# Kernel optimization log

Hardware: AMD Instinct MI355X
Metric: run time of the kernel (lower is better)

## Reference

```python
import jax, jax.numpy as jnp
import numpy as np

H, KVH, DH = 16, 4, 64
DIM = 1024
SCALE_BASE = 4096  # context_len
EPS = 1e-6


def rmsnorm(x, g):
    return x * jax.lax.rsqrt(jnp.mean(x * x, axis=-1, keepdims=True) + EPS) * g


def rope_tables(n, dh, dtype):
    inv_freq = 1.0 / (10000.0 ** (jnp.arange(0, dh, 2, dtype=jnp.float32) / dh))
    t = jnp.arange(n, dtype=jnp.float32) * (SCALE_BASE / n)
    freqs = t[:, None] * inv_freq[None, :]          # [n, dh/2]
    emb = jnp.concatenate([freqs, freqs], axis=-1)  # [n, dh]
    return jnp.cos(emb).astype(dtype), jnp.sin(emb).astype(dtype)


def apply_rope(x, cos, sin):
    # x: [b, h, n, dh]; cos/sin: [n, dh]
    x1, x2 = jnp.split(x, 2, axis=-1)
    rot = jnp.concatenate([-x2, x1], axis=-1)
    return x * cos + rot * sin


def setup_inputs() -> dict:
    key = jax.random.key(0)
    ks = jax.random.split(key, 12)
    B, N = 1, 2048
    std = 0.02
    inp = {
        "x": jax.random.normal(ks[0], (B, N, DIM), jnp.float32),
        "a": jax.random.normal(ks[1], (B, N, DIM), jnp.float32),
        "g_x": jnp.ones((DIM,), jnp.float32),
        "g_a": jnp.ones((DIM,), jnp.float32),
        "Wq_x": jax.random.normal(ks[2], (DIM, H * DH), jnp.float32) * std,
        "Wkv_x": jax.random.normal(ks[3], (DIM, 2 * KVH * DH), jnp.float32) * std,
        "Wq_a": jax.random.normal(ks[4], (DIM, H * DH), jnp.float32) * std,
        "Wkv_a": jax.random.normal(ks[5], (DIM, 2 * KVH * DH), jnp.float32) * std,
        "Wout_x": jax.random.normal(ks[6], (H * DH, DIM), jnp.float32) * std,
        "bout_x": jnp.zeros((DIM,), jnp.float32),
        "Wout_a": jax.random.normal(ks[7], (H * DH, DIM), jnp.float32) * std,
        "bout_a": jnp.zeros((DIM,), jnp.float32),
    }
    return inp


def _split_heads(t, h):
    b, n, hd = t.shape
    return t.reshape(b, n, h, hd // h).transpose(0, 2, 1, 3)  # b h n d


def _stream_qkv(s, g, Wq, Wkv):
    s = rmsnorm(s, g)
    q = _split_heads(s @ Wq, H)                 # [b, H, n, DH]
    kv = s @ Wkv
    k, v = jnp.split(kv, 2, axis=-1)
    k = _split_heads(k, KVH)                    # [b, KVH, n, DH]
    v = _split_heads(v, KVH)
    return q, k, v


def reference(x, a, g_x, g_a, Wq_x, Wkv_x, Wq_a, Wkv_a, Wout_x, bout_x, Wout_a, bout_a):
    B, Nx, _ = x.shape
    Na = a.shape[1]
    scale = DH ** -0.5
    r = H // KVH

    q_x, k_x, v_x = _stream_qkv(x, g_x, Wq_x, Wkv_x)
    q_a, k_a, v_a = _stream_qkv(a, g_a, Wq_a, Wkv_a)

    cos_x, sin_x = rope_tables(Nx, DH, x.dtype)
    cos_a, sin_a = rope_tables(Na, DH, a.dtype)
    q_x, k_x = apply_rope(q_x, cos_x, sin_x), apply_rope(k_x, cos_x, sin_x)
    q_a, k_a = apply_rope(q_a, cos_a, sin_a), apply_rope(k_a, cos_a, sin_a)

    # NOTE: original scales q by dim_head**-0.5 AND sdpa scales again -> 1/DH total
    q_x = q_x * scale
    q_a = q_a * scale

    # GQA expansion: einops 'b h n d -> b (r h) n d' == tile heads
    tile = lambda t: jnp.tile(t, (1, r, 1, 1))
    k_x, v_x, k_a, v_a = tile(k_x), tile(v_x), tile(k_a), tile(v_a)

    # pack [a, x] along seq
    q = jnp.concatenate([q_a, q_x], axis=2)
    k = jnp.concatenate([k_a, k_x], axis=2)
    v = jnp.concatenate([v_a, v_x], axis=2)

    scores = jnp.einsum('bhqd,bhkd->bhqk', q, k) * scale  # sdpa's own scale
    attn = jax.nn.softmax(scores, axis=-1)
    out = jnp.einsum('bhqk,bhkd->bhqd', attn, v)          # [b, H, Na+Nx, DH]

    out_a, out_x = out[:, :, :Na], out[:, :, Na:]
    merge = lambda t: t.transpose(0, 2, 1, 3).reshape(B, -1, H * DH)
    out_x = merge(out_x) @ Wout_x + bout_x
    out_a = merge(out_a) @ Wout_a + bout_a
    return out_x, out_a
```

## Files before the change

### kernel.cpp

```cpp
#include <hip/hip_runtime.h>
#include <hip/hip_bf16.h>
#include <stdint.h>
#include <math.h>


#define NSEQ 2048
#define NJ   4096
#define DIMM 1024
#define LPAD 72

typedef __attribute__((ext_vector_type(4))) float f32x4;
typedef __attribute__((ext_vector_type(8))) short bf16x8;
typedef __attribute__((ext_vector_type(4))) short bf16x4;

__device__ __forceinline__ unsigned short f2bf(float f) {
  union { float f; uint32_t u; } v; v.f = f;
  return (unsigned short)((v.u + 0x7FFFu + ((v.u >> 16) & 1u)) >> 16);
}

__device__ __forceinline__ uint32_t pack2bf(float a, float b) {
  __hip_bfloat162 h = __float22bfloat162_rn(float2{a, b});
  union { __hip_bfloat162 h; uint32_t u; } c; c.h = h;
  return c.u;
}

#if defined(__has_builtin)
#if __has_builtin(__builtin_amdgcn_exp2f)
#define FAST_EXP2(x) __builtin_amdgcn_exp2f(x)
#endif
#endif
#ifndef FAST_EXP2
#define FAST_EXP2(x) exp2f(x)
#endif

__device__ __forceinline__ void glds16(const void* g, void* l) {
  __builtin_amdgcn_global_load_lds(
      (const __attribute__((address_space(1))) unsigned int*)g,
      (__attribute__((address_space(3))) unsigned int*)l, 16, 0, 0);
}

__global__ __launch_bounds__(256) void prep_kernel(
    const float* __restrict__ xa, const float* __restrict__ xx,
    const float* __restrict__ ga, const float* __restrict__ gx,
    const float* __restrict__ wqa, const float* __restrict__ wqx,
    const float* __restrict__ wkva, const float* __restrict__ wkvx,
    const float* __restrict__ woa, const float* __restrict__ wox,
    unsigned short* __restrict__ XN, unsigned short* __restrict__ WQT,
    unsigned short* __restrict__ WKVT, unsigned short* __restrict__ WOT,
    float* __restrict__ cosT, float* __restrict__ sinT) {
  __shared__ float tile[32][33];
  __shared__ float red[4];
  int bid = blockIdx.x, t = threadIdx.x;
  if (bid < 256) {
    int idx = bid * 256 + t;
    int pos = idx >> 5, i = idx & 31;
    double inv = pow(10000.0, -(double)i / 32.0);
    double ang = (double)(2 * pos) * inv;
    cosT[idx] = (float)cos(ang);
    sinT[idx] = (float)sin(ang);
  } else if (bid < 6400) {
    int b = bid - 256;
    int z = b >> 10, yx = b & 1023;
    int n0 = (yx >> 5) * 32, k0 = (yx & 31) * 32;
    int s = z & 1, ty = z >> 1;
    int N = (ty == 1) ? 512 : 1024;
    if (n0 >= N) return;
    const float* src = (z == 0) ? wqa : (z == 1) ? wqx : (z == 2) ? wkva
                     : (z == 3) ? wkvx : (z == 4) ? woa : wox;
    unsigned short* dst = (ty == 0) ? WQT + (size_t)s * 1024 * 1024
                        : (ty == 1) ? WKVT + (size_t)s * 512 * 1024
                                    : WOT + (size_t)s * 1024 * 1024;
    int r = t >> 3, c4 = (t & 7) * 4;
    f32x4 v = *(const f32x4*)(src + (size_t)(k0 + r) * N + n0 + c4);
    tile[r][c4 + 0] = v.x; tile[r][c4 + 1] = v.y;
    tile[r][c4 + 2] = v.z; tile[r][c4 + 3] = v.w;
    __syncthreads();
    int nn = t >> 3, kk = (t & 7) * 4;
    bf16x4 o;
    o.x = (short)f2bf(tile[kk + 0][nn]);
    o.y = (short)f2bf(tile[kk + 1][nn]);
    o.z = (short)f2bf(tile[kk + 2][nn]);
    o.w = (short)f2bf(tile[kk + 3][nn]);
    *(bf16x4*)(dst + (size_t)(n0 + nn) * 1024 + k0 + kk) = o;
  } else {
    int b = bid - 6400;
    int s = b >> 11, row = b & 2047;
    const float* src = (s == 0 ? xa : xx) + (size_t)row * DIMM;
    const float* g = (s == 0 ? ga : gx);
    f32x4 v = *(const f32x4*)(src + t * 4);
    float ss = v.x * v.x + v.y * v.y + v.z * v.z + v.w * v.w;
#pragma unroll
    for (int o = 32; o > 0; o >>= 1) ss += __shfl_xor(ss, o, 64);
    if ((t & 63) == 0) red[t >> 6] = ss;
    __syncthreads();
    float tot = red[0] + red[1] + red[2] + red[3];
    float rs = rsqrtf(tot * (1.0f / DIMM) + 1e-6f);
    f32x4 gv = *(const f32x4*)(g + t * 4);
    bf16x4 o;
    o.x = (short)f2bf(v.x * rs * gv.x);
    o.y = (short)f2bf(v.y * rs * gv.y);
    o.z = (short)f2bf(v.z * rs * gv.z);
    o.w = (short)f2bf(v.w * rs * gv.w);
    *(bf16x4*)(XN + ((size_t)s * NSEQ + row) * DIMM + t * 4) = o;
  }
}

__device__ __forceinline__ void gemm128_mainloop(
    const unsigned short* __restrict__ Ag, const unsigned short* __restrict__ Bg,
    unsigned short* As, unsigned short* Bs, f32x4 acc[4][4]) {
  int t = threadIdx.x;
  int lane = t & 63, wid = t >> 6;
  int wm = (wid >> 1) * 64, wn = (wid & 1) * 64;
  int l15 = lane & 15, quad = lane >> 4;
  int srow = t >> 2, sko = (t & 3) * 8;
  const unsigned short* ga = Ag + (size_t)srow * 1024 + sko;
  const unsigned short* gb = Bg + (size_t)srow * 1024 + sko;
  unsigned short* la = As + t * 8;
  unsigned short* lb = Bs + t * 8;
#pragma unroll
  for (int mi = 0; mi < 4; ++mi)
#pragma unroll
    for (int j = 0; j < 4; ++j) acc[mi][j] = (f32x4){0.f, 0.f, 0.f, 0.f};
  for (int kt = 0; kt < 32; ++kt) {
    int k0 = kt * 32;
    __syncthreads();
    glds16(ga + k0, la);
    glds16(ga + 64 * 1024 + k0, la + 2048);
    glds16(gb + k0, lb);
    glds16(gb + 64 * 1024 + k0, lb + 2048);
    __syncthreads();
    bf16x8 af[4], bfr[4];
#pragma unroll
    for (int mi = 0; mi < 4; ++mi)
      af[mi] = *(const bf16x8*)(As + (wm + mi * 16 + l15) * 32 + quad * 8);
#pragma unroll
    for (int j = 0; j < 4; ++j)
      bfr[j] = *(const bf16x8*)(Bs + (wn + j * 16 + l15) * 32 + quad * 8);
#pragma unroll
    for (int mi = 0; mi < 4; ++mi)
#pragma unroll
      for (int j = 0; j < 4; ++j)
        acc[mi][j] = __builtin_amdgcn_mfma_f32_16x16x32_bf16(af[mi], bfr[j],
                                                             acc[mi][j], 0, 0, 0);
  }
}

__global__ __launch_bounds__(256) void gemm_qkv_kernel(
    const unsigned short* __restrict__ XN, const unsigned short* __restrict__ WQT,
    const unsigned short* __restrict__ WKVT, const float* __restrict__ cosT,
    const float* __restrict__ sinT, unsigned short* __restrict__ QB,
    unsigned short* __restrict__ KB, unsigned short* __restrict__ VT) {
  __shared__ unsigned short As[128 * 32], Bs[128 * 32];
  int n0 = blockIdx.x * 128, m0 = blockIdx.y * 128;
  int s = (m0 >= 2048) ? 1 : 0;
  const unsigned short* Ag = XN + (size_t)m0 * 1024;
  const unsigned short* Bg = (n0 < 1024)
      ? WQT + (size_t)s * 1024 * 1024 + (size_t)n0 * 1024
      : WKVT + (size_t)s * 512 * 1024 + (size_t)(n0 - 1024) * 1024;
  f32x4 acc[4][4];
  gemm128_mainloop(Ag, Bg, As, Bs, acc);
  int t = threadIdx.x, lane = t & 63, wid = t >> 6;
  int wm = (wid >> 1) * 64, wn = (wid & 1) * 64;
  int l15 = lane & 15, quad = lane >> 4;
  int coln = n0 + wn;
  if (coln < 1280) {
    bool isq = coln < 1024;
    float sc = isq ? (1.4426950408889634f / 64.0f) : 1.0f;
    unsigned short* dstBase;
    if (isq) dstBase = QB + (size_t)(coln >> 6) * NJ * 64;
    else     dstBase = KB + (size_t)((coln - 1024) >> 6) * NJ * 64;
#pragma unroll
    for (int mi = 0; mi < 4; ++mi)
#pragma unroll
      for (int r = 0; r < 4; ++r) {
        int jr = m0 + wm + mi * 16 + quad * 4 + r;
        int pos = jr & 2047;
#pragma unroll
        for (int jp = 0; jp < 2; ++jp) {
          int i = jp * 16 + l15;
          float c = cosT[pos * 32 + i], sn = sinT[pos * 32 + i];
          float x1 = acc[mi][jp][r], x2 = acc[mi][jp + 2][r];
          dstBase[(size_t)jr * 64 + jp * 16 + l15]      = f2bf((x1 * c - x2 * sn) * sc);
          dstBase[(size_t)jr * 64 + 32 + jp * 16 + l15] = f2bf((x2 * c + x1 * sn) * sc);
        }
      }
  } else {
    int cvb = coln - 1280;
#pragma unroll
    for (int mi = 0; mi < 4; ++mi)
#pragma unroll
      for (int j = 0; j < 4; ++j) {
        int d = cvb + j * 16 + l15;
        int jr0 = m0 + wm + mi * 16 + quad * 4;
        union { bf16x4 v; uint32_t u[2]; } pv;
        pv.u[0] = pack2bf(acc[mi][j][0], acc[mi][j][1]);
        pv.u[1] = pack2bf(acc[mi][j][2], acc[mi][j][3]);
        *(bf16x4*)(VT + (size_t)d * NJ + jr0) = pv.v;
      }
  }
}

__global__ __launch_bounds__(256, 4) void attn_kernel(
    const unsigned short* __restrict__ QB, const unsigned short* __restrict__ KB,
    const unsigned short* __restrict__ VT, unsigned short* __restrict__ AT) {
  __shared__ unsigned short Ks[2][64 * LPAD];
  __shared__ unsigned short Vs[2][64 * LPAD];
  int h = blockIdx.y, qt = blockIdx.x;
  int hk = h & 3;
  int t = threadIdx.x, lane = t & 63, w = t >> 6;
  int l15 = lane & 15, quad = lane >> 4;
  int q0 = qt * 128 + w * 16;
  bf16x8 qf[2][2];
#pragma unroll
  for (int mi = 0; mi < 2; ++mi) {
    const unsigned short* qp = QB + ((size_t)h * NJ + q0 + mi * 64 + l15) * 64;
    qf[mi][0] = *(const bf16x8*)(qp + quad * 8);
    qf[mi][1] = *(const bf16x8*)(qp + 32 + quad * 8);
  }
  f32x4 oT[2][4];
  f32x4 oL[2];
#pragma unroll
  for (int mi = 0; mi < 2; ++mi) {
    oL[mi] = (f32x4){0.f, 0.f, 0.f, 0.f};
#pragma unroll
    for (int db = 0; db < 4; ++db) oT[mi][db] = (f32x4){0.f, 0.f, 0.f, 0.f};
  }
  bf16x8 vone;
  {
    short one = (l15 == 0) ? (short)0x3F80 : (short)0;
    vone = (bf16x8){one, one, one, one, one, one, one, one};
  }
  const unsigned short* Kg = KB + (size_t)hk * NJ * 64;
  const unsigned short* Vg = VT + (size_t)hk * 64 * NJ;
  int ky = t >> 3, dof = (t & 7) * 8;
  int pky = (ky & 0x23) | ((ky & 0x18) >> 1) | ((ky & 0x04) << 2);
  const unsigned short* KgA = Kg + (size_t)ky * 64 + dof;
  const unsigned short* KgB = Kg + (size_t)(32 + ky) * 64 + dof;
  const unsigned short* VgA = Vg + (size_t)ky * NJ + dof;
  const unsigned short* VgB = Vg + (size_t)(32 + ky) * NJ + dof;
  bf16x8 kr0 = *(const bf16x8*)(KgA);
  bf16x8 kr1 = *(const bf16x8*)(KgB);
  bf16x8 vr0 = *(const bf16x8*)(VgA);
  bf16x8 vr1 = *(const bf16x8*)(VgB);
  *(bf16x8*)(Ks[0] + pky * LPAD + dof) = kr0;
  *(bf16x8*)(Ks[0] + (32 + pky) * LPAD + dof) = kr1;
  *(bf16x8*)(Vs[0] + ky * LPAD + dof) = vr0;
  *(bf16x8*)(Vs[0] + (32 + ky) * LPAD + dof) = vr1;
  kr0 = *(const bf16x8*)(KgA + 4096);
  kr1 = *(const bf16x8*)(KgB + 4096);
  vr0 = *(const bf16x8*)(VgA + 64);
  vr1 = *(const bf16x8*)(VgB + 64);
  __syncthreads();
  for (int kt = 0; kt < 64; ++kt) {
    int cur = kt & 1;
    unsigned short* Kd = Ks[cur ^ 1];
    unsigned short* Vd = Vs[cur ^ 1];
    *(bf16x8*)(Kd + pky * LPAD + dof) = kr0;
    *(bf16x8*)(Kd + (32 + pky) * LPAD + dof) = kr1;
    *(bf16x8*)(Vd + ky * LPAD + dof) = vr0;
    *(bf16x8*)(Vd + (32 + ky) * LPAD + dof) = vr1;
    int tn = (kt + 2) & 63;
    kr0 = *(const bf16x8*)(KgA + (size_t)tn * 4096);
    kr1 = *(const bf16x8*)(KgB + (size_t)tn * 4096);
    vr0 = *(const bf16x8*)(VgA + tn * 64);
    vr1 = *(const bf16x8*)(VgB + tn * 64);
    const unsigned short* Kc = Ks[cur];
    const unsigned short* Vc = Vs[cur];
    f32x4 sx[2][4];
#pragma unroll
    for (int jb = 0; jb < 4; ++jb) {
      const unsigned short* kp = Kc + (jb * 16 + l15) * LPAD;
      bf16x8 kf0 = *(const bf16x8*)(kp + quad * 8);
      bf16x8 kf1 = *(const bf16x8*)(kp + 32 + quad * 8);
      f32x4 z0 = (f32x4){0.f, 0.f, 0.f, 0.f};
      z0 = __builtin_amdgcn_mfma_f32_16x16x32_bf16(kf0, qf[0][0], z0, 0, 0, 0);
      z0 = __builtin_amdgcn_mfma_f32_16x16x32_bf16(kf1, qf[0][1], z0, 0, 0, 0);
      sx[0][jb] = z0;
      f32x4 z1 = (f32x4){0.f, 0.f, 0.f, 0.f};
      z1 = __builtin_amdgcn_mfma_f32_16x16x32_bf16(kf0, qf[1][0], z1, 0, 0, 0);
      z1 = __builtin_amdgcn_mfma_f32_16x16x32_bf16(kf1, qf[1][1], z1, 0, 0, 0);
      sx[1][jb] = z1;
    }
    bf16x8 pb[2][2];
#pragma unroll
    for (int mi = 0; mi < 2; ++mi)
#pragma unroll
      for (int sb = 0; sb < 2; ++sb) {
        union { bf16x8 v; uint32_t u[4]; } pk;
        pk.u[0] = pack2bf(FAST_EXP2(sx[mi][2 * sb][0]), FAST_EXP2(sx[mi][2 * sb][1]));
        pk.u[1] = pack2bf(FAST_EXP2(sx[mi][2 * sb][2]), FAST_EXP2(sx[mi][2 * sb][3]));
        pk.u[2] = pack2bf(FAST_EXP2(sx[mi][2 * sb + 1][0]), FAST_EXP2(sx[mi][2 * sb + 1][1]));
        pk.u[3] = pack2bf(FAST_EXP2(sx[mi][2 * sb + 1][2]), FAST_EXP2(sx[mi][2 * sb + 1][3]));
        pb[mi][sb] = pk.v;
      }
#pragma unroll
    for (int db = 0; db < 4; ++db)
#pragma unroll
      for (int sb = 0; sb < 2; ++sb) {
        bf16x8 va = *(const bf16x8*)(Vc + (db * 16 + l15) * LPAD + sb * 32 + quad * 8);
        oT[0][db] = __builtin_amdgcn_mfma_f32_16x16x32_bf16(va, pb[0][sb],
                                                            oT[0][db], 0, 0, 0);
        oT[1][db] = __builtin_amdgcn_mfma_f32_16x16x32_bf16(va, pb[1][sb],
                                                            oT[1][db], 0, 0, 0);
      }
#pragma unroll
    for (int mi = 0; mi < 2; ++mi)
#pragma unroll
      for (int sb = 0; sb < 2; ++sb)
        oL[mi] = __builtin_amdgcn_mfma_f32_16x16x32_bf16(vone, pb[mi][sb],
                                                         oL[mi], 0, 0, 0);
    __syncthreads();
  }
#pragma unroll
  for (int mi = 0; mi < 2; ++mi) {
    float s = oL[mi][0];
    s += __shfl_xor(s, 16, 64);
    s += __shfl_xor(s, 32, 64);
    float inv = 1.0f / s;
    int qrow = q0 + mi * 64 + l15;
#pragma unroll
    for (int db = 0; db < 4; ++db) {
      union { bf16x4 v; uint32_t u[2]; } ov;
      ov.u[0] = pack2bf(oT[mi][db][0] * inv, oT[mi][db][1] * inv);
      ov.u[1] = pack2bf(oT[mi][db][2] * inv, oT[mi][db][3] * inv);
      *(bf16x4*)(AT + (size_t)qrow * DIMM + h * 64 + db * 16 + quad * 4) = ov.v;
    }
  }
}

__global__ __launch_bounds__(256) void gemm_out_kernel(
    const unsigned short* __restrict__ AT, const unsigned short* __restrict__ WOT,
    const float* __restrict__ ba, const float* __restrict__ bx,
    float* __restrict__ out) {
  __shared__ unsigned short As[128 * 32], Bs[128 * 32];
  int n0 = blockIdx.x * 128, m0 = blockIdx.y * 128;
  int s = (m0 >= 2048) ? 1 : 0;
  const unsigned short* Ag = AT + (size_t)m0 * 1024;
  const unsigned short* Bg = WOT + (size_t)s * 1024 * 1024 + (size_t)n0 * 1024;
  f32x4 acc[4][4];
  gemm128_mainloop(Ag, Bg, As, Bs, acc);
  int t = threadIdx.x, lane = t & 63, wid = t >> 6;
  int wm = (wid >> 1) * 64, wn = (wid & 1) * 64;
  int l15 = lane & 15, quad = lane >> 4;
  const float* bias = s ? bx : ba;
  float* obase = s ? (out + (size_t)(m0 - 2048) * 1024)
                   : (out + (size_t)2048 * 1024 + (size_t)m0 * 1024);
#pragma unroll
  for (int mi = 0; mi < 4; ++mi)
#pragma unroll
    for (int r = 0; r < 4; ++r) {
      int row = wm + mi * 16 + quad * 4 + r;
#pragma unroll
      for (int j = 0; j < 4; ++j) {
        int col = n0 + wn + j * 16 + l15;
        obase[(size_t)row * 1024 + col] = acc[mi][j][r] + bias[col];
      }
    }
}

extern "C" void kernel_launch(void* const* d_in, const int* in_sizes, int n_in,
                              void* d_out, int out_size, void* d_ws, size_t ws_size,
                              hipStream_t stream) {
  const float* x      = (const float*)d_in[0];
  const float* a      = (const float*)d_in[1];
  const float* g_x    = (const float*)d_in[2];
  const float* g_a    = (const float*)d_in[3];
  const float* Wq_x   = (const float*)d_in[4];
  const float* Wkv_x  = (const float*)d_in[5];
  const float* Wq_a   = (const float*)d_in[6];
  const float* Wkv_a  = (const float*)d_in[7];
  const float* Wout_x = (const float*)d_in[8];
  const float* bout_x = (const float*)d_in[9];
  const float* Wout_a = (const float*)d_in[10];
  const float* bout_a = (const float*)d_in[11];
  float* out = (float*)d_out;

  char* ws = (char*)d_ws;
  const size_t MB = 1024 * 1024;
  unsigned short* XN   = (unsigned short*)(ws);
  unsigned short* WQT  = (unsigned short*)(ws + 8 * MB);
  unsigned short* WKVT = (unsigned short*)(ws + 12 * MB);
  unsigned short* WOT  = (unsigned short*)(ws + 14 * MB);
  unsigned short* QB   = (unsigned short*)(ws + 18 * MB);
  unsigned short* KB   = (unsigned short*)(ws + 26 * MB);
  unsigned short* VT   = (unsigned short*)(ws + 28 * MB);
  float* cosT          = (float*)(ws + 30 * MB);
  float* sinT          = (float*)(ws + 30 * MB + 262144);
  unsigned short* AT   = XN;

  prep_kernel<<<dim3(10496), dim3(256), 0, stream>>>(
      a, x, g_a, g_x, Wq_a, Wq_x, Wkv_a, Wkv_x, Wout_a, Wout_x,
      XN, WQT, WKVT, WOT, cosT, sinT);
  gemm_qkv_kernel<<<dim3(12, 32), dim3(256), 0, stream>>>(
      XN, WQT, WKVT, cosT, sinT, QB, KB, VT);
  attn_kernel<<<dim3(32, 16), dim3(256), 0, stream>>>(QB, KB, VT, AT);
  gemm_out_kernel<<<dim3(8, 32), dim3(256), 0, stream>>>(
      AT, WOT, bout_a, bout_x, out);
}
```

Baseline: 227.3 us.

## Split attention KV tile across warp pairs with LDS reduction of partial outputs

Each warp now handles 64 query rows against half of every 64-key tile, instead of 32 query rows against the whole tile. Each K and V fragment read from LDS then feeds four MFMA query blocks rather than two, which cuts LDS read traffic per MFMA. Partial outputs and row sums from the two key halves are combined through shared memory at the end. The cost is twice the accumulator registers, so the occupancy hint in launch bounds is lowered from 4 to 2, plus an extra barrier and reduction step.

```diff
diff --git a/kernel.cpp b/kernel.cpp
--- a/kernel.cpp
+++ b/kernel.cpp
@@ -200,27 +200,28 @@
   }
 }
 
-__global__ __launch_bounds__(256, 4) void attn_kernel(
+__global__ __launch_bounds__(256, 2) void attn_kernel(
     const unsigned short* __restrict__ QB, const unsigned short* __restrict__ KB,
     const unsigned short* __restrict__ VT, unsigned short* __restrict__ AT) {
-  __shared__ unsigned short Ks[2][64 * LPAD];
-  __shared__ unsigned short Vs[2][64 * LPAD];
+  __shared__ __align__(16) unsigned short Ks[2][64 * LPAD];
+  __shared__ __align__(16) unsigned short Vs[2][64 * LPAD];
   int h = blockIdx.y, qt = blockIdx.x;
   int hk = h & 3;
   int t = threadIdx.x, lane = t & 63, w = t >> 6;
   int l15 = lane & 15, quad = lane >> 4;
-  int q0 = qt * 128 + w * 16;
-  bf16x8 qf[2][2];
-#pragma unroll
-  for (int mi = 0; mi < 2; ++mi) {
-    const unsigned short* qp = QB + ((size_t)h * NJ + q0 + mi * 64 + l15) * 64;
+  int qsel = w >> 1, ksel = w & 1;
+  int q0 = qt * 128 + qsel * 64;
+  bf16x8 qf[4][2];
+#pragma unroll
+  for (int mi = 0; mi < 4; ++mi) {
+    const unsigned short* qp = QB + ((size_t)h * NJ + q0 + mi * 16 + l15) * 64;
     qf[mi][0] = *(const bf16x8*)(qp + quad * 8);
     qf[mi][1] = *(const bf16x8*)(qp + 32 + quad * 8);
   }
-  f32x4 oT[2][4];
-  f32x4 oL[2];
-#pragma unroll
-  for (int mi = 0; mi < 2; ++mi) {
+  f32x4 oT[4][4];
+  f32x4 oL[4];
+#pragma unroll
+  for (int mi = 0; mi < 4; ++mi) {
     oL[mi] = (f32x4){0.f, 0.f, 0.f, 0.f};
 #pragma unroll
     for (int db = 0; db < 4; ++db) oT[mi][db] = (f32x4){0.f, 0.f, 0.f, 0.f};
@@ -266,64 +267,80 @@
     vr1 = *(const bf16x8*)(VgB + tn * 64);
     const unsigned short* Kc = Ks[cur];
     const unsigned short* Vc = Vs[cur];
-    f32x4 sx[2][4];
-#pragma unroll
-    for (int jb = 0; jb < 4; ++jb) {
+    f32x4 sx[4][2];
+#pragma unroll
+    for (int jj = 0; jj < 2; ++jj) {
+      int jb = 2 * ksel + jj;
       const unsigned short* kp = Kc + (jb * 16 + l15) * LPAD;
       bf16x8 kf0 = *(const bf16x8*)(kp + quad * 8);
       bf16x8 kf1 = *(const bf16x8*)(kp + 32 + quad * 8);
-      f32x4 z0 = (f32x4){0.f, 0.f, 0.f, 0.f};
-      z0 = __builtin_amdgcn_mfma_f32_16x16x32_bf16(kf0, qf[0][0], z0, 0, 0, 0);
-      z0 = __builtin_amdgcn_mfma_f32_16x16x32_bf16(kf1, qf[0][1], z0, 0, 0, 0);
-      sx[0][jb] = z0;
-      f32x4 z1 = (f32x4){0.f, 0.f, 0.f, 0.f};
-      z1 = __builtin_amdgcn_mfma_f32_16x16x32_bf16(kf0, qf[1][0], z1, 0, 0, 0);
-      z1 = __builtin_amdgcn_mfma_f32_16x16x32_bf16(kf1, qf[1][1], z1, 0, 0, 0);
-      sx[1][jb] = z1;
+#pragma unroll
+      for (int mi = 0; mi < 4; ++mi) {
+        f32x4 z = (f32x4){0.f, 0.f, 0.f, 0.f};
+        z = __builtin_amdgcn_mfma_f32_16x16x32_bf16(kf0, qf[mi][0], z, 0, 0, 0);
+        z = __builtin_amdgcn_mfma_f32_16x16x32_bf16(kf1, qf[mi][1], z, 0, 0, 0);
+        sx[mi][jj] = z;
+      }
     }
-    bf16x8 pb[2][2];
-#pragma unroll
-    for (int mi = 0; mi < 2; ++mi)
-#pragma unroll
-      for (int sb = 0; sb < 2; ++sb) {
-        union { bf16x8 v; uint32_t u[4]; } pk;
-        pk.u[0] = pack2bf(FAST_EXP2(sx[mi][2 * sb][0]), FAST_EXP2(sx[mi][2 * sb][1]));
-        pk.u[1] = pack2bf(FAST_EXP2(sx[mi][2 * sb][2]), FAST_EXP2(sx[mi][2 * sb][3]));
-        pk.u[2] = pack2bf(FAST_EXP2(sx[mi][2 * sb + 1][0]), FAST_EXP2(sx[mi][2 * sb + 1][1]));
-        pk.u[3] = pack2bf(FAST_EXP2(sx[mi][2 * sb + 1][2]), FAST_EXP2(sx[mi][2 * sb + 1][3]));
-        pb[mi][sb] = pk.v;
-      }
-#pragma unroll
-    for (int db = 0; db < 4; ++db)
-#pragma unroll
-      for (int sb = 0; sb < 2; ++sb) {
-        bf16x8 va = *(const bf16x8*)(Vc + (db * 16 + l15) * LPAD + sb * 32 + quad * 8);
-        oT[0][db] = __builtin_amdgcn_mfma_f32_16x16x32_bf16(va, pb[0][sb],
-                                                            oT[0][db], 0, 0, 0);
-        oT[1][db] = __builtin_amdgcn_mfma_f32_16x16x32_bf16(va, pb[1][sb],
-                                                            oT[1][db], 0, 0, 0);
-      }
-#pragma unroll
-    for (int mi = 0; mi < 2; ++mi)
-#pragma unroll
-      for (int sb = 0; sb < 2; ++sb)
-        oL[mi] = __builtin_amdgcn_mfma_f32_16x16x32_bf16(vone, pb[mi][sb],
-                                                         oL[mi], 0, 0, 0);
+    bf16x8 pb[4];
+#pragma unroll
+    for (int mi = 0; mi < 4; ++mi) {
+      union { bf16x8 v; uint32_t u[4]; } pk;
+      pk.u[0] = pack2bf(FAST_EXP2(sx[mi][0][0]), FAST_EXP2(sx[mi][0][1]));
+      pk.u[1] = pack2bf(FAST_EXP2(sx[mi][0][2]), FAST_EXP2(sx[mi][0][3]));
+      pk.u[2] = pack2bf(FAST_EXP2(sx[mi][1][0]), FAST_EXP2(sx[mi][1][1]));
+      pk.u[3] = pack2bf(FAST_EXP2(sx[mi][1][2]), FAST_EXP2(sx[mi][1][3]));
+      pb[mi] = pk.v;
+    }
+#pragma unroll
+    for (int db = 0; db < 4; ++db) {
+      bf16x8 va = *(const bf16x8*)(Vc + (db * 16 + l15) * LPAD + ksel * 32 + quad * 8);
+#pragma unroll
+      for (int mi = 0; mi < 4; ++mi)
+        oT[mi][db] = __builtin_amdgcn_mfma_f32_16x16x32_bf16(va, pb[mi],
+                                                             oT[mi][db], 0, 0, 0);
+    }
+#pragma unroll
+    for (int mi = 0; mi < 4; ++mi)
+      oL[mi] = __builtin_amdgcn_mfma_f32_16x16x32_bf16(vone, pb[mi],
+                                                       oL[mi], 0, 0, 0);
     __syncthreads();
   }
-#pragma unroll
-  for (int mi = 0; mi < 2; ++mi) {
+  float ls[4];
+#pragma unroll
+  for (int mi = 0; mi < 4; ++mi) {
     float s = oL[mi][0];
     s += __shfl_xor(s, 16, 64);
     s += __shfl_xor(s, 32, 64);
-    float inv = 1.0f / s;
-    int qrow = q0 + mi * 64 + l15;
-#pragma unroll
-    for (int db = 0; db < 4; ++db) {
-      union { bf16x4 v; uint32_t u[2]; } ov;
-      ov.u[0] = pack2bf(oT[mi][db][0] * inv, oT[mi][db][1] * inv);
-      ov.u[1] = pack2bf(oT[mi][db][2] * inv, oT[mi][db][3] * inv);
-      *(bf16x4*)(AT + (size_t)qrow * DIMM + h * 64 + db * 16 + quad * 4) = ov.v;
+    ls[mi] = s;
+  }
+  float* xb = (float*)(qsel == 0 ? &Ks[0][0] : &Vs[0][0]);
+  if (ksel == 1) {
+    f32x4* dst = (f32x4*)xb + (size_t)lane * 16;
+#pragma unroll
+    for (int mi = 0; mi < 4; ++mi)
+#pragma unroll
+      for (int db = 0; db < 4; ++db) dst[mi * 4 + db] = oT[mi][db];
+    float* dl = xb + 64 * 64 + lane * 4;
+#pragma unroll
+    for (int mi = 0; mi < 4; ++mi) dl[mi] = ls[mi];
+  }
+  __syncthreads();
+  if (ksel == 0) {
+    const f32x4* src = (const f32x4*)xb + (size_t)lane * 16;
+    const float* sl = xb + 64 * 64 + lane * 4;
+#pragma unroll
+    for (int mi = 0; mi < 4; ++mi) {
+      float inv = 1.0f / (ls[mi] + sl[mi]);
+      int qrow = q0 + mi * 16 + l15;
+#pragma unroll
+      for (int db = 0; db < 4; ++db) {
+        f32x4 o = oT[mi][db] + src[mi * 4 + db];
+        union { bf16x4 v; uint32_t u[2]; } ov;
+        ov.u[0] = pack2bf(o[0] * inv, o[1] * inv);
+        ov.u[1] = pack2bf(o[2] * inv, o[3] * inv);
+        *(bf16x4*)(AT + (size_t)qrow * DIMM + h * 64 + db * 16 + quad * 4) = ov.v;
+      }
     }
   }
 }
```

New measurement: 225.0 us. No clear change (-1.0%).
